# Optimization experiments

Hardware: AMD Instinct MI355X
Metric: run time of the kernel (lower is better)

Reference implementation:

```python
import jax, jax.numpy as jnp
import numpy as np

IN_DIM, HIDDEN, OUT_DIM = 784, 2048, 10
BATCH = 16384
KEEP = 0.1  # 1 - sparsity


def setup_inputs() -> dict:
    key = jax.random.key(0)
    ks = jax.random.split(key, 16)
    s1 = 1.0 / np.sqrt(IN_DIM)
    sh = 1.0 / np.sqrt(HIDDEN)
    inp = {
        "x": jax.random.normal(ks[0], (BATCH, IN_DIM), dtype=jnp.float32),
        # weights stored as (out, in) like nn.Linear
        "W1": jax.random.uniform(ks[1], (HIDDEN, IN_DIM), jnp.float32, -s1, s1),
        "b1": jax.random.uniform(ks[2], (HIDDEN,), jnp.float32, -s1, s1),
        "W2": jax.random.uniform(ks[3], (HIDDEN, HIDDEN), jnp.float32, -sh, sh),
        "b2": jax.random.uniform(ks[4], (HIDDEN,), jnp.float32, -sh, sh),
        "W3": jax.random.uniform(ks[5], (HIDDEN, HIDDEN), jnp.float32, -sh, sh),
        "b3": jax.random.uniform(ks[6], (HIDDEN,), jnp.float32, -sh, sh),
        "W4": jax.random.uniform(ks[7], (HIDDEN, HIDDEN), jnp.float32, -sh, sh),
        "b4": jax.random.uniform(ks[8], (HIDDEN,), jnp.float32, -sh, sh),
        "W5": jax.random.uniform(ks[9], (OUT_DIM, HIDDEN), jnp.float32, -sh, sh),
        "b5": jax.random.uniform(ks[10], (OUT_DIM,), jnp.float32, -sh, sh),
        "m1": jax.random.bernoulli(ks[11], KEEP, (HIDDEN, IN_DIM)),
        "m2": jax.random.bernoulli(ks[12], KEEP, (HIDDEN, HIDDEN)),
        "m3": jax.random.bernoulli(ks[13], KEEP, (HIDDEN, HIDDEN)),
        "m4": jax.random.bernoulli(ks[14], KEEP, (HIDDEN, HIDDEN)),
    }
    return inp


def _sparse_linear(x, W, b, m):
    # masked linear: y = x @ (W*m)^T + b
    Wm = W * m.astype(W.dtype)
    return x @ Wm.T + b


def reference(x, W1, b1, W2, b2, W3, b3, W4, b4, W5, b5, m1, m2, m3, m4):
    h = x.reshape(x.shape[0], -1)
    h = jax.nn.relu(_sparse_linear(h, W1, b1, m1))
    h = jax.nn.relu(_sparse_linear(h, W2, b2, m2))
    h = jax.nn.relu(_sparse_linear(h, W3, b3, m3))
    h = jax.nn.relu(_sparse_linear(h, W4, b4, m4))
    return h @ W5.T + b5
```

## Files before the change

kernel.cpp:

```cpp
#include <hip/hip_runtime.h>
#include <hip/hip_bf16.h>
#include <hip/hip_fp16.h>

#define BATCH 16384
#define HID   2048
#define IND   784
#define INDP  896
#define OUTD  10

typedef _Float16 f16;
typedef __attribute__((ext_vector_type(8))) _Float16 f16x8;
typedef __attribute__((ext_vector_type(4))) float f32x4;

__global__ void mask_detect(const unsigned char* __restrict__ p, int nbytes,
                            int* __restrict__ flags) {
    int acc = 0;
    for (int i = blockIdx.x * blockDim.x + threadIdx.x; i < nbytes;
         i += gridDim.x * blockDim.x) {
        unsigned char b = p[i];
        if (b > 1) acc |= 2;
        else if (b != 0 && (i & 3) != 0) acc |= 1;
    }
    if (acc) atomicOr(flags, acc);
}

__global__ void prep_cast(const float* __restrict__ W,
                          const void* __restrict__ Mk,
                          const int* __restrict__ flags,
                          f16* __restrict__ out,
                          int rin, int kin, int kout, int total) {
    int idx = blockIdx.x * blockDim.x + threadIdx.x;
    if (idx >= total) return;
    int r = idx / kout, c = idx - r * kout;
    float v = 0.f;
    if (r < rin && c < kin) {
        v = W[(size_t)r * kin + c];
        if (Mk) {
            size_t mi = (size_t)r * kin + c;
            bool byteMode = (*flags == 1);
            bool keep = byteMode ? (((const unsigned char*)Mk)[mi] != 0)
                                 : (((const unsigned int*)Mk)[mi] != 0u);
            if (!keep) v = 0.f;
        }
    }
    out[idx] = (f16)v;
}

__device__ __forceinline__ void gload_lds16(const f16* g, f16* l) {
    __builtin_amdgcn_global_load_lds(
        (const __attribute__((address_space(1))) unsigned int*)g,
        (__attribute__((address_space(3))) unsigned int*)l,
        16, 0, 0);
}

#define BAR()    __builtin_amdgcn_s_barrier()
#define SCHED()  __builtin_amdgcn_sched_barrier(0)
#define WAITV4() asm volatile("s_waitcnt vmcnt(4)" ::: "memory")
#define WAITV8() asm volatile("s_waitcnt vmcnt(8)" ::: "memory")

template<bool RELU>
__global__ __launch_bounds__(512, 2) void gemm8p(
    const f16* __restrict__ A, const f16* __restrict__ B,
    const float* __restrict__ bias, f16* __restrict__ C,
    int N, int K) {
    __shared__ f16 As[2 * 2 * 256 * 32];
    __shared__ f16 Bs[2 * 2 * 256 * 32];

    int nbn = N >> 8;
    int nwg = gridDim.x;
    int cpx = nwg >> 3;
    int bid = blockIdx.x;
    int swz = (bid & 7) * cpx + (bid >> 3);
    int bm = swz / nbn, bn = swz % nbn;

    int tid = threadIdx.x;
    int w = tid >> 6, lane = tid & 63;
    int wr = w >> 2, wc = w & 3;
    int l15 = lane & 15, l4 = lane >> 4;

    const f16* Ag = A + (size_t)bm * 256 * K;
    const f16* Bg = B + (size_t)bn * 256 * K;

    int r0 = tid >> 2, s0 = tid & 3;
    int c0 = (s0 ^ ((r0 >> 1) & 3)) * 8;
    int ldsw0 = (w * 64) * 8;
    int ldsw1 = (512 + w * 64) * 8;

    auto stageA = [&](int buf, int ks, int tk) {
        gload_lds16(Ag + (size_t)r0 * K + tk * 64 + ks * 32 + c0,
                    As + (buf * 2 + ks) * 8192 + ldsw0);
        gload_lds16(Ag + (size_t)(128 + r0) * K + tk * 64 + ks * 32 + c0,
                    As + (buf * 2 + ks) * 8192 + ldsw1);
    };
    auto stageB = [&](int buf, int ks, int tk) {
        gload_lds16(Bg + (size_t)r0 * K + tk * 64 + ks * 32 + c0,
                    Bs + (buf * 2 + ks) * 8192 + ldsw0);
        gload_lds16(Bg + (size_t)(128 + r0) * K + tk * 64 + ks * 32 + c0,
                    Bs + (buf * 2 + ks) * 8192 + ldsw1);
    };

    int rsw = (l4 ^ ((l15 >> 1) & 3)) * 8;
    auto ldA = [&](f16x8 (&af)[4], int buf, int ks, int mh) {
        int base = (buf * 2 + ks) * 8192;
        #pragma unroll
        for (int m = 0; m < 4; ++m) {
            int row = wr * 128 + (mh * 4 + m) * 16 + l15;
            af[m] = *(const f16x8*)(As + base + row * 32 + rsw);
        }
    };
    auto ldB = [&](f16x8 (&bf)[4], int buf, int ks) {
        int base = (buf * 2 + ks) * 8192;
        #pragma unroll
        for (int n = 0; n < 4; ++n) {
            int row = wc * 64 + n * 16 + l15;
            bf[n] = *(const f16x8*)(Bs + base + row * 32 + rsw);
        }
    };

    f32x4 acc[8][4] = {};
    auto mma = [&](f16x8 (&af)[4], f16x8 (&bf)[4], int mh) {
        __builtin_amdgcn_s_setprio(1);
        #pragma unroll
        for (int m = 0; m < 4; ++m)
            #pragma unroll
            for (int n = 0; n < 4; ++n)
                acc[mh * 4 + m][n] = __builtin_amdgcn_mfma_f32_16x16x32_f16(
                    af[m], bf[n], acc[mh * 4 + m][n], 0, 0, 0);
        __builtin_amdgcn_s_setprio(0);
    };

    int NT = K >> 6, NI = NT >> 1;

    f16x8 Aa[4], Ab[4], Ba[4], Bb[4];

    stageA(0, 0, 0); stageB(0, 0, 0); stageA(0, 1, 0); stageB(0, 1, 0);
    stageA(1, 0, 1); stageB(1, 0, 1);
    WAITV8(); SCHED(); BAR();
    ldA(Aa, 0, 0, 0); ldB(Bb, 0, 0); ldA(Ab, 0, 0, 1);
    WAITV4(); SCHED(); BAR();

    for (int it = 0; it < NI; ++it) {
        int t1 = 2 * it + 1, t2 = 2 * it + 2, t3 = 2 * it + 3;
        if (t2 >= NT) t2 = 0;
        if (t3 >= NT) t3 = 0;

        mma(Aa, Bb, 0); SCHED();
        ldA(Aa, 0, 1, 0); ldB(Ba, 0, 1); stageA(1, 1, t1);
        SCHED(); BAR();
        mma(Ab, Bb, 1); SCHED();
        ldA(Ab, 0, 1, 1); stageB(1, 1, t1);
        WAITV4(); SCHED(); BAR();
        mma(Aa, Ba, 0); SCHED();
        ldA(Aa, 1, 0, 0); ldB(Bb, 1, 0); stageA(0, 0, t2);
        SCHED(); BAR();
        mma(Ab, Ba, 1); SCHED();
        ldA(Ab, 1, 0, 1); stageB(0, 0, t2);
        WAITV4(); SCHED(); BAR();
        mma(Aa, Bb, 0); SCHED();
        ldA(Aa, 1, 1, 0); ldB(Ba, 1, 1); stageA(0, 1, t2);
        SCHED(); BAR();
        mma(Ab, Bb, 1); SCHED();
        ldA(Ab, 1, 1, 1); stageB(0, 1, t2);
        WAITV4(); SCHED(); BAR();
        mma(Aa, Ba, 0); SCHED();
        ldA(Aa, 0, 0, 0); ldB(Bb, 0, 0); stageA(1, 0, t3);
        SCHED(); BAR();
        mma(Ab, Ba, 1); SCHED();
        ldA(Ab, 0, 0, 1); stageB(1, 0, t3);
        WAITV4(); SCHED(); BAR();
    }

    #pragma unroll
    for (int nf = 0; nf < 4; ++nf) {
        int j = bn * 256 + wc * 64 + nf * 16 + l15;
        float bv = bias[j];
        #pragma unroll
        for (int mf = 0; mf < 8; ++mf) {
            int i0 = bm * 256 + wr * 128 + mf * 16 + l4 * 4;
            #pragma unroll
            for (int r = 0; r < 4; ++r) {
                float v = acc[mf][nf][r] + bv;
                if (RELU) v = fmaxf(v, 0.f);
                C[(size_t)(i0 + r) * N + j] = (f16)v;
            }
        }
    }
}

__global__ __launch_bounds__(256, 3) void gemm_head(
    const f16* __restrict__ A, const f16* __restrict__ B,
    const float* __restrict__ bias, float* __restrict__ C,
    int K, int Nout) {
    __shared__ f16 As[128 * 64];
    __shared__ f16 Bs[128 * 64];
    int bm = blockIdx.x;
    int t = threadIdx.x;
    int w = t >> 6, lane = t & 63;
    int wm = w >> 1, wn = w & 1;
    int l15 = lane & 15, l4 = lane >> 4;
    const f16* Ag = A + (size_t)bm * 128 * K;
    const f16* Bg = B;
    int rr = w * 8 + (lane >> 3);
    int cc = (lane & 7) * 8;
    f32x4 acc[4][4] = {};
    for (int k0 = 0; k0 < K; k0 += 64) {
        #pragma unroll
        for (int i = 0; i < 4; ++i)
            gload_lds16(Ag + (size_t)(i * 32 + rr) * K + k0 + cc, As + i * 2048 + w * 512);
        #pragma unroll
        for (int i = 0; i < 4; ++i)
            gload_lds16(Bg + (size_t)(i * 32 + rr) * K + k0 + cc, Bs + i * 2048 + w * 512);
        __syncthreads();
        #pragma unroll
        for (int ks = 0; ks < 2; ++ks) {
            f16x8 af[4], bfr[4];
            #pragma unroll
            for (int m = 0; m < 4; ++m)
                af[m] = *(const f16x8*)(As + (wm * 64 + m * 16 + l15) * 64 + ks * 32 + l4 * 8);
            #pragma unroll
            for (int n = 0; n < 4; ++n)
                bfr[n] = *(const f16x8*)(Bs + (wn * 64 + n * 16 + l15) * 64 + ks * 32 + l4 * 8);
            #pragma unroll
            for (int m = 0; m < 4; ++m)
                #pragma unroll
                for (int n = 0; n < 4; ++n)
                    acc[m][n] = __builtin_amdgcn_mfma_f32_16x16x32_f16(af[m], bfr[n], acc[m][n], 0, 0, 0);
        }
        __syncthreads();
    }
    #pragma unroll
    for (int n = 0; n < 4; ++n) {
        int j = wn * 64 + n * 16 + l15;
        bool jok = j < Nout;
        float bv = jok ? bias[j] : 0.f;
        #pragma unroll
        for (int m = 0; m < 4; ++m) {
            int i0 = bm * 128 + wm * 64 + m * 16 + l4 * 4;
            #pragma unroll
            for (int r = 0; r < 4; ++r) {
                if (jok) C[(size_t)(i0 + r) * Nout + j] = acc[m][n][r] + bv;
            }
        }
    }
}

extern "C" void kernel_launch(void* const* d_in, const int* in_sizes, int n_in,
                              void* d_out, int out_size, void* d_ws, size_t ws_size,
                              hipStream_t stream) {
    const float* x  = (const float*)d_in[0];
    const float* W1 = (const float*)d_in[1];
    const float* b1 = (const float*)d_in[2];
    const float* W2 = (const float*)d_in[3];
    const float* b2 = (const float*)d_in[4];
    const float* W3 = (const float*)d_in[5];
    const float* b3 = (const float*)d_in[6];
    const float* W4 = (const float*)d_in[7];
    const float* b4 = (const float*)d_in[8];
    const float* W5 = (const float*)d_in[9];
    const float* b5 = (const float*)d_in[10];
    const void* m1 = d_in[11];
    const void* m2 = d_in[12];
    const void* m3 = d_in[13];
    const void* m4 = d_in[14];

    char* ws = (char*)d_ws;
    size_t off = 0;
    auto alloc = [&](size_t b) { char* p = ws + off; off += (b + 255) & ~(size_t)255; return p; };
    f16* xb  = (f16*)alloc((size_t)BATCH * INDP * 2);
    f16* w1b = (f16*)alloc((size_t)HID * INDP * 2);
    f16* w2b = (f16*)alloc((size_t)HID * HID * 2);
    f16* w3b = (f16*)alloc((size_t)HID * HID * 2);
    f16* w4b = (f16*)alloc((size_t)HID * HID * 2);
    f16* w5b = (f16*)alloc((size_t)128 * HID * 2);
    f16* h1  = (f16*)alloc((size_t)BATCH * HID * 2);
    f16* h2  = (f16*)alloc((size_t)BATCH * HID * 2);
    int* flags = (int*)alloc(256);

    hipMemsetAsync(flags, 0, sizeof(int), stream);
    mask_detect<<<64, 256, 0, stream>>>((const unsigned char*)m1, 262144, flags);

    auto prep = [&](const float* src, const void* mk, f16* dst,
                    int rin, int kin, int kout, int rout) {
        int total = rout * kout;
        prep_cast<<<(total + 255) / 256, 256, 0, stream>>>(src, mk, flags, dst,
                                                           rin, kin, kout, total);
    };
    prep(x,  nullptr, xb,  BATCH, IND, INDP, BATCH);
    prep(W1, m1,      w1b, HID,   IND, INDP, HID);
    prep(W2, m2,      w2b, HID,   HID, HID,  HID);
    prep(W3, m3,      w3b, HID,   HID, HID,  HID);
    prep(W4, m4,      w4b, HID,   HID, HID,  HID);
    prep(W5, nullptr, w5b, OUTD,  HID, HID,  128);

    int g8 = (BATCH / 256) * (HID / 256);
    gemm8p<true><<<g8, 512, 0, stream>>>(xb, w1b, b1, h1, HID, INDP);
    gemm8p<true><<<g8, 512, 0, stream>>>(h1, w2b, b2, h2, HID, HID);
    gemm8p<true><<<g8, 512, 0, stream>>>(h2, w3b, b3, h1, HID, HID);
    gemm8p<true><<<g8, 512, 0, stream>>>(h1, w4b, b4, h2, HID, HID);
    gemm_head<<<BATCH / 128, 256, 0, stream>>>(h2, w5b, b5, (float*)d_out, HID, OUTD);
}
```

Before: 538.9 us.

## Vectorize weight/input cast kernel and relax scheduling barriers after MFMA

Replaces the scalar prep_cast kernel with a version where each thread handles four elements, using float4 loads for weights and activations and uchar4/uint4 loads for masks. This cuts instruction count and improves memory coalescing in the preprocessing passes over x and the weight matrices. It also removes the sched_barrier that followed each mma call in the GEMM main loop, so the compiler can interleave the LDS reads and global-to-LDS staging with the MFMAs. That may improve overlap, but it gives up the explicitly controlled instruction schedule.

```diff
diff --git a/kernel.cpp b/kernel.cpp
--- a/kernel.cpp
+++ b/kernel.cpp
@@ -10,6 +10,7 @@
 
 typedef _Float16 f16;
 typedef __attribute__((ext_vector_type(8))) _Float16 f16x8;
+typedef __attribute__((ext_vector_type(4))) _Float16 f16x4;
 typedef __attribute__((ext_vector_type(4))) float f32x4;
 
 __global__ void mask_detect(const unsigned char* __restrict__ p, int nbytes,
@@ -24,26 +25,33 @@
     if (acc) atomicOr(flags, acc);
 }
 
-__global__ void prep_cast(const float* __restrict__ W,
-                          const void* __restrict__ Mk,
-                          const int* __restrict__ flags,
-                          f16* __restrict__ out,
-                          int rin, int kin, int kout, int total) {
+__global__ void prep_cast4(const float* __restrict__ W,
+                           const void* __restrict__ Mk,
+                           const int* __restrict__ flags,
+                           f16* __restrict__ out,
+                           int rin, int kin, int kout, int total4) {
     int idx = blockIdx.x * blockDim.x + threadIdx.x;
-    if (idx >= total) return;
-    int r = idx / kout, c = idx - r * kout;
-    float v = 0.f;
+    if (idx >= total4) return;
+    int k4 = kout >> 2;
+    int r = idx / k4, c = (idx - r * k4) << 2;
+    f16x4 o = {};
     if (r < rin && c < kin) {
-        v = W[(size_t)r * kin + c];
+        float4 v = *(const float4*)(W + (size_t)r * kin + c);
+        float vv0 = v.x, vv1 = v.y, vv2 = v.z, vv3 = v.w;
         if (Mk) {
-            size_t mi = (size_t)r * kin + c;
-            bool byteMode = (*flags == 1);
-            bool keep = byteMode ? (((const unsigned char*)Mk)[mi] != 0)
-                                 : (((const unsigned int*)Mk)[mi] != 0u);
-            if (!keep) v = 0.f;
-        }
-    }
-    out[idx] = (f16)v;
+            if (*flags == 1) {
+                uchar4 m = *(const uchar4*)((const unsigned char*)Mk + (size_t)r * kin + c);
+                if (!m.x) vv0 = 0.f; if (!m.y) vv1 = 0.f;
+                if (!m.z) vv2 = 0.f; if (!m.w) vv3 = 0.f;
+            } else {
+                uint4 m = *(const uint4*)((const unsigned int*)Mk + (size_t)r * kin + c);
+                if (!m.x) vv0 = 0.f; if (!m.y) vv1 = 0.f;
+                if (!m.z) vv2 = 0.f; if (!m.w) vv3 = 0.f;
+            }
+        }
+        o[0] = (f16)vv0; o[1] = (f16)vv1; o[2] = (f16)vv2; o[3] = (f16)vv3;
+    }
+    *(f16x4*)(out + (size_t)r * kout + c) = o;
 }
 
 __device__ __forceinline__ void gload_lds16(const f16* g, f16* l) {
@@ -144,28 +152,28 @@
         if (t2 >= NT) t2 = 0;
         if (t3 >= NT) t3 = 0;
 
-        mma(Aa, Bb, 0); SCHED();
+        mma(Aa, Bb, 0);
         ldA(Aa, 0, 1, 0); ldB(Ba, 0, 1); stageA(1, 1, t1);
         SCHED(); BAR();
-        mma(Ab, Bb, 1); SCHED();
+        mma(Ab, Bb, 1);
         ldA(Ab, 0, 1, 1); stageB(1, 1, t1);
         WAITV4(); SCHED(); BAR();
-        mma(Aa, Ba, 0); SCHED();
+        mma(Aa, Ba, 0);
         ldA(Aa, 1, 0, 0); ldB(Bb, 1, 0); stageA(0, 0, t2);
         SCHED(); BAR();
-        mma(Ab, Ba, 1); SCHED();
+        mma(Ab, Ba, 1);
         ldA(Ab, 1, 0, 1); stageB(0, 0, t2);
         WAITV4(); SCHED(); BAR();
-        mma(Aa, Bb, 0); SCHED();
+        mma(Aa, Bb, 0);
         ldA(Aa, 1, 1, 0); ldB(Ba, 1, 1); stageA(0, 1, t2);
         SCHED(); BAR();
-        mma(Ab, Bb, 1); SCHED();
+        mma(Ab, Bb, 1);
         ldA(Ab, 1, 1, 1); stageB(0, 1, t2);
         WAITV4(); SCHED(); BAR();
-        mma(Aa, Ba, 0); SCHED();
+        mma(Aa, Ba, 0);
         ldA(Aa, 0, 0, 0); ldB(Bb, 0, 0); stageA(1, 0, t3);
         SCHED(); BAR();
-        mma(Ab, Ba, 1); SCHED();
+        mma(Ab, Ba, 1);
         ldA(Ab, 0, 0, 1); stageB(1, 0, t3);
         WAITV4(); SCHED(); BAR();
     }
@@ -281,9 +289,9 @@
 
     auto prep = [&](const float* src, const void* mk, f16* dst,
                     int rin, int kin, int kout, int rout) {
-        int total = rout * kout;
-        prep_cast<<<(total + 255) / 256, 256, 0, stream>>>(src, mk, flags, dst,
-                                                           rin, kin, kout, total);
+        int total4 = rout * (kout >> 2);
+        prep_cast4<<<(total4 + 255) / 256, 256, 0, stream>>>(src, mk, flags, dst,
+                                                             rin, kin, kout, total4);
     };
     prep(x,  nullptr, xb,  BATCH, IND, INDP, BATCH);
     prep(W1, m1,      w1b, HID,   IND, INDP, HID);
```

Result: faster. 514.4 us (-4.5%).
